# Kernel optimization log

Hardware: AMD Instinct MI355X
Metric: run time of the kernel (lower is better)

Reference implementation:

```python
import jax, jax.numpy as jnp
import numpy as np

B, V = 8, 60000

def _embed(x, n):
    # NeRF positional encoding: [x, sin(x*2^0), cos(x*2^0), ..., sin(x*2^{n-1}), cos(x*2^{n-1})]
    f = 2.0 ** jnp.arange(n, dtype=x.dtype)
    xf = x[..., None, :] * f[:, None]                      # [..., n, D]
    sc = jnp.stack([jnp.sin(xf), jnp.cos(xf)], axis=-2)    # [..., n, 2, D] (per-freq sin/cos interleave)
    return jnp.concatenate([x, sc.reshape(x.shape[:-1] + (-1,))], axis=-1)

def _mlp(x, params):
    for W, b in params[:-1]:
        x = jax.nn.silu(x @ W.T + b)
    W, b = params[-1]
    return x @ W.T + b

def _rx(a):
    c, s = jnp.cos(a), jnp.sin(a)
    o, z = jnp.ones_like(a), jnp.zeros_like(a)
    return jnp.stack([jnp.stack([o, z, z], -1), jnp.stack([z, c, -s], -1), jnp.stack([z, s, c], -1)], -2)

def _ry(a):
    c, s = jnp.cos(a), jnp.sin(a)
    o, z = jnp.ones_like(a), jnp.zeros_like(a)
    return jnp.stack([jnp.stack([c, z, s], -1), jnp.stack([z, o, z], -1), jnp.stack([-s, z, c], -1)], -2)

def _rz(a):
    c, s = jnp.cos(a), jnp.sin(a)
    o, z = jnp.ones_like(a), jnp.zeros_like(a)
    return jnp.stack([jnp.stack([c, -s, z], -1), jnp.stack([s, c, z], -1), jnp.stack([z, z, o], -1)], -2)

def _forward(vertices, features, ew0, eb0, ew1, eb1, ew2, eb2, ew3, eb3, ew4, eb4, ew5, eb5,
             tw0, tb0, tw1, tb1, tw2, tb2, tw3, tb3,
             pw0, pb0, pw1, pb1, pw2, pb2, pw3, pb3,
             transform_origin, scale):
    enc_v = _embed(vertices, 6)                            # [V, 78]
    enc_ov = _embed(vertices[:, :3], 3)                    # [V, 21]
    tmpl = _mlp(enc_ov, [(tw0, tb0), (tw1, tb1), (tw2, tb2), (tw3, tb3)])  # [V, 3]
    di = jnp.concatenate([jnp.broadcast_to(enc_v[None], (B, V, enc_v.shape[-1])),
                          jnp.broadcast_to(features[:, None, :53], (B, V, 53))], -1)  # [B,V,131]
    expr = _mlp(di, [(ew0, eb0), (ew1, eb1), (ew2, eb2), (ew3, eb3), (ew4, eb4), (ew5, eb5)])  # [B,V,3]
    ev = vertices[None, :, :3] + expr + tmpl[None]         # [B, V, 3]
    pi = jnp.concatenate([jnp.broadcast_to(enc_ov[None], (B, V, enc_ov.shape[-1])),
                          jnp.broadcast_to(features[:, None, 53:59], (B, V, 6))], -1)  # [B,V,27]
    w = jax.nn.sigmoid(_mlp(pi, [(pw0, pb0), (pw1, pb1), (pw2, pb2), (pw3, pb3)]))  # [B,V,1]
    ang = features[:, None, 53:56] * w                     # [B,V,3] per-vertex scaled euler angles
    # pytorch3d euler_angles_to_matrix, convention 'XYZ': R = R_X @ R_Y @ R_Z
    R = _rx(ang[..., 0]) @ _ry(ang[..., 1]) @ _rz(ang[..., 2])  # [B,V,3,3]
    origin = transform_origin * 0.1
    local = (ev - origin) * scale
    return jnp.einsum('bvd,bvdj->bvj', local, R) + features[:, None, 56:59] + origin

def _lin(key, fi, fo):
    # mimics xavier_uniform_(gain=0.1) + zero bias
    lim = 0.1 * np.sqrt(6.0 / (fi + fo))
    W = jax.random.uniform(key, (fo, fi), minval=-lim, maxval=lim, dtype=jnp.float32)
    return W, jnp.zeros((fo,), jnp.float32)

def setup_inputs():
    key = jax.random.key(0)
    ks = jax.random.split(key, 20)
    d = {}
    d['vertices'] = jax.random.normal(ks[0], (V, 6), jnp.float32)
    d['features'] = jax.random.normal(ks[1], (B, 62), jnp.float32) * 0.3
    exp_dims = [(131, 256), (256, 256), (256, 128), (128, 128), (128, 128), (128, 3)]
    for i, (fi, fo) in enumerate(exp_dims):
        d['ew%d' % i], d['eb%d' % i] = _lin(ks[2 + i], fi, fo)
    tmpl_dims = [(21, 64), (64, 32), (32, 32), (32, 3)]
    for i, (fi, fo) in enumerate(tmpl_dims):
        d['tw%d' % i], d['tb%d' % i] = _lin(ks[8 + i], fi, fo)
    pose_dims = [(27, 64), (64, 32), (32, 32), (32, 1)]
    for i, (fi, fo) in enumerate(pose_dims):
        d['pw%d' % i], d['pb%d' % i] = _lin(ks[12 + i], fi, fo)
    d['transform_origin'] = jnp.zeros((3,), jnp.float32)
    d['scale'] = jnp.ones((1,), jnp.float32)
    return d

def reference(vertices, features, ew0, eb0, ew1, eb1, ew2, eb2, ew3, eb3, ew4, eb4, ew5, eb5,
              tw0, tb0, tw1, tb1, tw2, tb2, tw3, tb3,
              pw0, pb0, pw1, pb1, pw2, pb2, pw3, pb3,
              transform_origin, scale):
    return _forward(vertices, features, ew0, eb0, ew1, eb1, ew2, eb2, ew3, eb3, ew4, eb4, ew5, eb5,
                    tw0, tb0, tw1, tb1, tw2, tb2, tw3, tb3,
                    pw0, pb0, pw1, pb1, pw2, pb2, pw3, pb3,
                    transform_origin, scale)
```

## Files before the change

kernel.cpp:

```cpp
#include <hip/hip_runtime.h>
#include <hip/hip_bf16.h>
#include <math.h>

#define V_TOT 60000
#define VPB 8
#define NBLK (V_TOT / VPB)

typedef short  s16x8 __attribute__((ext_vector_type(8)));
typedef float  f32x4 __attribute__((ext_vector_type(4)));

#define WS_EW0 0
#define WS_EW1 40960
#define WS_EW2 106496
#define WS_EW3 139264
#define WS_EW4 155648
#define WS_EW5 172032
#define WS_PW0 174080
#define WS_PW1 176128
#define WS_PW2 178176
#define WS_PW3 179200
#define WS_TW0 179712
#define WS_TW1 181760
#define WS_TW2 183808
#define WS_TW3 184832

#define L_ACTA 0
#define L_ENCF 0
#define L_OENC 2560
#define L_ACTB 33792
#define L_PH0  33792
#define L_PH1  43008
#define L_PH2  48128
#define L_A0P  67584
#define L_A0T  71680
#define L_TA   72704
#define L_TB   75008
#define L_TC   76288
#define L_FEAT 77568
#define L_VERT 79552
#define L_EXPR 79744
#define L_TMPL 80512
#define L_POSW 80608
#define SMEM_BYTES 80864

struct Params {
  const float* vertices; const float* features;
  const float* eb0; const float* eb1; const float* eb2; const float* eb3;
  const float* eb4; const float* eb5;
  const float* tb0; const float* tb1; const float* tb2; const float* tb3;
  const float* pb0; const float* pb1; const float* pb2; const float* pb3;
  const float* torigin; const float* scale;
  const ushort* wsb;
  float* out;
};

__device__ __forceinline__ float silu_f(float x) {
  float e = __expf(-x);
  return x * __builtin_amdgcn_rcpf(1.f + e);
}
__device__ __forceinline__ float sigm_f(float x) {
  return __builtin_amdgcn_rcpf(1.f + __expf(-x));
}
__device__ __forceinline__ ushort f2bf(float f) {
  unsigned u = __float_as_uint(f);
  return (ushort)((u + 0x7fffu + ((u >> 16) & 1u)) >> 16);
}
__device__ __forceinline__ unsigned pack2bf(float a, float b) {
  __hip_bfloat162 h = __float22bfloat162_rn(float2{a, b});
  unsigned u; __builtin_memcpy(&u, &h, 4); return u;
}

template<int KS, int SLOTS, int INSTR, int OUTSTR>
__device__ __forceinline__ void big_layer_T(const ushort* __restrict__ Wt,
                                            const float* __restrict__ bias,
                                            const ushort* inb, ushort* outb,
                                            int lane, int wv)
{
  const int r16 = lane & 15, g = lane >> 4;
  f32x4 acc[SLOTS][4];
  #pragma unroll
  for (int s = 0; s < SLOTS; s++) {
    const int nt = wv + s * 8;
    const float4 bv = *(const float4*)(bias + nt * 16 + g * 4);
    #pragma unroll
    for (int mt = 0; mt < 4; mt++) acc[s][mt] = (f32x4){bv.x, bv.y, bv.z, bv.w};
  }
  #pragma unroll
  for (int k = 0; k < KS; k++) {
    s16x8 bf[4];
    #pragma unroll
    for (int mt = 0; mt < 4; mt++)
      bf[mt] = *(const s16x8*)(inb + (mt * 16 + r16) * INSTR + k * 32 + g * 8);
    #pragma unroll
    for (int s = 0; s < SLOTS; s++) {
      const int nt = wv + s * 8;
      s16x8 aw = *(const s16x8*)(Wt + (size_t)(nt * KS + k) * 512 + lane * 8);
      #pragma unroll
      for (int mt = 0; mt < 4; mt++)
        acc[s][mt] = __builtin_amdgcn_mfma_f32_16x16x32_bf16(aw, bf[mt], acc[s][mt], 0, 0, 0);
    }
  }
  #pragma unroll
  for (int s = 0; s < SLOTS; s++) {
    const int nt = wv + s * 8;
    #pragma unroll
    for (int mt = 0; mt < 4; mt++) {
      uint2 w;
      w.x = pack2bf(silu_f(acc[s][mt][0]), silu_f(acc[s][mt][1]));
      w.y = pack2bf(silu_f(acc[s][mt][2]), silu_f(acc[s][mt][3]));
      *(uint2*)(outb + (mt * 16 + r16) * OUTSTR + nt * 16 + g * 4) = w;
    }
  }
}

template<int KS, int INSTR>
__device__ __forceinline__ f32x4 tile_mm_T(const ushort* __restrict__ Wt,
                                           const ushort* inb, int mt, int lane, f32x4 binit)
{
  const int r16 = lane & 15, g = lane >> 4;
  f32x4 acc = binit;
  #pragma unroll
  for (int k = 0; k < KS; k++) {
    s16x8 aw = *(const s16x8*)(Wt + k * 512 + lane * 8);
    s16x8 bf = *(const s16x8*)(inb + (mt * 16 + r16) * INSTR + k * 32 + g * 8);
    acc = __builtin_amdgcn_mfma_f32_16x16x32_bf16(aw, bf, acc, 0, 0, 0);
  }
  return acc;
}

__global__ void conv_w(const float* __restrict__ src, ushort* __restrict__ dst,
                       int NT, int KS, int Ksrc, int Kused, int Nused)
{
  int idx = blockIdx.x * 256 + threadIdx.x;
  if (idx >= NT * KS * 512) return;
  int t = idx >> 9, l = (idx >> 3) & 63, i = idx & 7;
  int nt = t / KS, k = t - nt * KS;
  int row = nt * 16 + (l & 15);
  int kk = k * 32 + (l >> 4) * 8 + i;
  float v = (row < Nused && kk < Kused) ? src[row * Ksrc + kk] : 0.f;
  dst[idx] = f2bf(v);
}

extern "C" __global__ __launch_bounds__(512, 4)
void nbs_kernel(Params P)
{
  extern __shared__ char sm[];
  ushort* actAb = (ushort*)(sm + L_ACTA);
  float*  encf  = (float*)(sm + L_ENCF);
  float*  oencf = (float*)(sm + L_OENC);
  ushort* a0    = (ushort*)(sm + L_ACTB);
  ushort* actBb = (ushort*)(sm + L_ACTB);
  ushort* ph0b  = (ushort*)(sm + L_PH0);
  ushort* ph1b  = (ushort*)(sm + L_PH1);
  ushort* ph2b  = (ushort*)(sm + L_PH2);
  ushort* a0p   = (ushort*)(sm + L_A0P);
  ushort* a0t   = (ushort*)(sm + L_A0T);
  ushort* tAl   = (ushort*)(sm + L_TA);
  ushort* tBl   = (ushort*)(sm + L_TB);
  ushort* tCl   = (ushort*)(sm + L_TC);
  float*  featl = (float*)(sm + L_FEAT);
  float*  vertl = (float*)(sm + L_VERT);
  float*  exprv = (float*)(sm + L_EXPR);
  float*  tmplv = (float*)(sm + L_TMPL);
  float*  posew = (float*)(sm + L_POSW);

  const int tid  = threadIdx.x;
  const int lane = tid & 63;
  const int wv   = __builtin_amdgcn_readfirstlane(tid >> 6);
  const int r16  = lane & 15, g = lane >> 4;
  const int v0   = blockIdx.x * VPB;
  const ushort* ws = P.wsb;

  for (int idx = tid; idx < 8 * 62; idx += 512) featl[idx] = P.features[idx];
  for (int idx = tid; idx < VPB * 6; idx += 512) vertl[idx] = P.vertices[(size_t)v0 * 6 + idx];
  __syncthreads();

  for (int idx = tid; idx < 8 * 80; idx += 512) {
    int v = idx / 80, e = idx - v * 80;
    float val = 0.f;
    if (e < 6) val = vertl[v * 6 + e];
    else if (e < 78) {
      int r = e - 6, k = r / 12, q = r - k * 12;
      float x = vertl[v * 6 + (q < 6 ? q : q - 6)] * (float)(1 << k);
      val = (q < 6) ? __sinf(x) : __cosf(x);
    }
    encf[idx] = val;
  }
  for (int idx = tid; idx < 8 * 24; idx += 512) {
    int v = idx / 24, e = idx - v * 24;
    float val = 0.f;
    if (e < 3) val = vertl[v * 6 + e];
    else if (e < 21) {
      int r = e - 3, k = r / 6, q = r - k * 6;
      float x = vertl[v * 6 + (q < 3 ? q : q - 3)] * (float)(1 << k);
      val = (q < 3) ? __sinf(x) : __cosf(x);
    }
    oencf[idx] = val;
  }
  __syncthreads();

  {
    uint* a0u = (uint*)a0;
    for (int idx = tid; idx < 64 * 80; idx += 512) {
      int p = idx / 80, q = idx - p * 80, vl = p >> 3, b = p & 7;
      int e0 = q * 2, e1 = e0 + 1;
      float s0 = (e0 < 78) ? encf[vl * 80 + e0] : (e0 < 131 ? featl[b * 62 + e0 - 78] : 0.f);
      float s1 = (e1 < 78) ? encf[vl * 80 + e1] : (e1 < 131 ? featl[b * 62 + e1 - 78] : 0.f);
      a0u[p * 80 + q] = pack2bf(s0, s1);
    }
    uint* a0pu = (uint*)a0p;
    for (int idx = tid; idx < 64 * 16; idx += 512) {
      int p = idx >> 4, q = idx & 15, vl = p >> 3, b = p & 7;
      int e0 = q * 2, e1 = e0 + 1;
      float s0 = (e0 < 21) ? oencf[vl * 24 + e0] : (e0 < 27 ? featl[b * 62 + 53 + e0 - 21] : 0.f);
      float s1 = (e1 < 21) ? oencf[vl * 24 + e1] : (e1 < 27 ? featl[b * 62 + 53 + e1 - 21] : 0.f);
      a0pu[p * 16 + q] = pack2bf(s0, s1);
    }
    uint* a0tu = (uint*)a0t;
    for (int idx = tid; idx < 16 * 16; idx += 512) {
      int v = idx >> 4, q = idx & 15;
      int e0 = q * 2, e1 = e0 + 1;
      float s0 = (v < 8 && e0 < 21) ? oencf[v * 24 + e0] : 0.f;
      float s1 = (v < 8 && e1 < 21) ? oencf[v * 24 + e1] : 0.f;
      a0tu[v * 16 + q] = pack2bf(s0, s1);
    }
  }
  __syncthreads();

  big_layer_T<5, 2, 160, 264>(ws + WS_EW0, P.eb0, a0,    actAb, lane, wv);
  __syncthreads();
  big_layer_T<8, 2, 264, 264>(ws + WS_EW1, P.eb1, actAb, actBb, lane, wv);
  __syncthreads();
  big_layer_T<8, 1, 264, 264>(ws + WS_EW2, P.eb2, actBb, actAb, lane, wv);
  __syncthreads();
  big_layer_T<4, 1, 264, 264>(ws + WS_EW3, P.eb3, actAb, actBb, lane, wv);
  __syncthreads();
  big_layer_T<4, 1, 264, 264>(ws + WS_EW4, P.eb4, actBb, actAb, lane, wv);
  __syncthreads();

  if (wv < 4) {
    const int nt = wv;
    const float4 bv = *(const float4*)(P.pb0 + nt * 16 + g * 4);
    #pragma unroll
    for (int mt = 0; mt < 4; mt++) {
      f32x4 d = tile_mm_T<1, 32>(ws + WS_PW0 + nt * 512, a0p, mt, lane,
                                 (f32x4){bv.x, bv.y, bv.z, bv.w});
      uint2 w;
      w.x = pack2bf(silu_f(d[0]), silu_f(d[1]));
      w.y = pack2bf(silu_f(d[2]), silu_f(d[3]));
      *(uint2*)(ph0b + (mt * 16 + r16) * 72 + nt * 16 + g * 4) = w;
    }
  } else {
    const int nt = wv - 4;
    const float4 bv = *(const float4*)(P.tb0 + nt * 16 + g * 4);
    f32x4 d = tile_mm_T<1, 32>(ws + WS_TW0 + nt * 512, a0t, 0, lane,
                               (f32x4){bv.x, bv.y, bv.z, bv.w});
    uint2 w;
    w.x = pack2bf(silu_f(d[0]), silu_f(d[1]));
    w.y = pack2bf(silu_f(d[2]), silu_f(d[3]));
    *(uint2*)(tAl + r16 * 72 + nt * 16 + g * 4) = w;
  }
  __syncthreads();

  if (wv >= 4) {
    const int mt = wv - 4;
    f32x4 bi = (f32x4){0.f, 0.f, 0.f, 0.f};
    if (g == 0) bi = (f32x4){P.eb5[0], P.eb5[1], P.eb5[2], 0.f};
    f32x4 d = tile_mm_T<4, 264>(ws + WS_EW5, actAb, mt, lane, bi);
    if (g == 0) {
      exprv[(mt * 16 + r16) * 3 + 0] = d[0];
      exprv[(mt * 16 + r16) * 3 + 1] = d[1];
      exprv[(mt * 16 + r16) * 3 + 2] = d[2];
    }
  } else if (wv < 2) {
    const int nt = wv;
    const float4 bv = *(const float4*)(P.pb1 + nt * 16 + g * 4);
    #pragma unroll
    for (int mt = 0; mt < 4; mt++) {
      f32x4 d = tile_mm_T<2, 72>(ws + WS_PW1 + nt * 2 * 512, ph0b, mt, lane,
                                 (f32x4){bv.x, bv.y, bv.z, bv.w});
      uint2 w;
      w.x = pack2bf(silu_f(d[0]), silu_f(d[1]));
      w.y = pack2bf(silu_f(d[2]), silu_f(d[3]));
      *(uint2*)(ph1b + (mt * 16 + r16) * 40 + nt * 16 + g * 4) = w;
    }
  } else {
    const int nt = wv - 2;
    const float4 bv = *(const float4*)(P.tb1 + nt * 16 + g * 4);
    f32x4 d = tile_mm_T<2, 72>(ws + WS_TW1 + nt * 2 * 512, tAl, 0, lane,
                               (f32x4){bv.x, bv.y, bv.z, bv.w});
    uint2 w;
    w.x = pack2bf(silu_f(d[0]), silu_f(d[1]));
    w.y = pack2bf(silu_f(d[2]), silu_f(d[3]));
    *(uint2*)(tBl + r16 * 40 + nt * 16 + g * 4) = w;
  }
  __syncthreads();

  if (wv < 2) {
    const int nt = wv;
    const float4 bv = *(const float4*)(P.pb2 + nt * 16 + g * 4);
    #pragma unroll
    for (int mt = 0; mt < 4; mt++) {
      f32x4 d = tile_mm_T<1, 40>(ws + WS_PW2 + nt * 512, ph1b, mt, lane,
                                 (f32x4){bv.x, bv.y, bv.z, bv.w});
      uint2 w;
      w.x = pack2bf(silu_f(d[0]), silu_f(d[1]));
      w.y = pack2bf(silu_f(d[2]), silu_f(d[3]));
      *(uint2*)(ph2b + (mt * 16 + r16) * 40 + nt * 16 + g * 4) = w;
    }
  } else if (wv == 2) {
    #pragma unroll
    for (int nt = 0; nt < 2; nt++) {
      const float4 bv = *(const float4*)(P.tb2 + nt * 16 + g * 4);
      f32x4 d = tile_mm_T<1, 40>(ws + WS_TW2 + nt * 512, tBl, 0, lane,
                                 (f32x4){bv.x, bv.y, bv.z, bv.w});
      uint2 w;
      w.x = pack2bf(silu_f(d[0]), silu_f(d[1]));
      w.y = pack2bf(silu_f(d[2]), silu_f(d[3]));
      *(uint2*)(tCl + r16 * 40 + nt * 16 + g * 4) = w;
    }
  }
  __syncthreads();

  if (wv == 0) {
    f32x4 bi = (g == 0) ? (f32x4){P.pb3[0], 0.f, 0.f, 0.f} : (f32x4){0.f, 0.f, 0.f, 0.f};
    #pragma unroll
    for (int mt = 0; mt < 4; mt++) {
      f32x4 d = tile_mm_T<1, 40>(ws + WS_PW3, ph2b, mt, lane, bi);
      if (g == 0) posew[mt * 16 + r16] = sigm_f(d[0]);
    }
  } else if (wv == 1) {
    f32x4 bi = (g == 0) ? (f32x4){P.tb3[0], P.tb3[1], P.tb3[2], 0.f}
                        : (f32x4){0.f, 0.f, 0.f, 0.f};
    f32x4 d = tile_mm_T<1, 40>(ws + WS_TW3, tCl, 0, lane, bi);
    if (g == 0 && r16 < 8) {
      tmplv[r16 * 3 + 0] = d[0];
      tmplv[r16 * 3 + 1] = d[1];
      tmplv[r16 * 3 + 2] = d[2];
    }
  }
  __syncthreads();

  if (tid < 64) {
    int p = tid, vl = p >> 3, b = p & 7;
    float ox = P.torigin[0] * 0.1f, oy = P.torigin[1] * 0.1f, oz = P.torigin[2] * 0.1f;
    float sc = P.scale[0];
    float ev0 = vertl[vl * 6 + 0] + exprv[p * 3 + 0] + tmplv[vl * 3 + 0];
    float ev1 = vertl[vl * 6 + 1] + exprv[p * 3 + 1] + tmplv[vl * 3 + 1];
    float ev2 = vertl[vl * 6 + 2] + exprv[p * 3 + 2] + tmplv[vl * 3 + 2];
    float w = posew[p];
    float a0a = featl[b * 62 + 53] * w;
    float a1a = featl[b * 62 + 54] * w;
    float a2a = featl[b * 62 + 55] * w;
    float c1 = __cosf(a0a), s1 = __sinf(a0a);
    float c2 = __cosf(a1a), s2 = __sinf(a1a);
    float c3 = __cosf(a2a), s3 = __sinf(a2a);
    float R00 = c2 * c3,                R01 = -c2 * s3,                R02 = s2;
    float R10 = c1 * s3 + s1 * s2 * c3, R11 = c1 * c3 - s1 * s2 * s3,  R12 = -s1 * c2;
    float R20 = s1 * s3 - c1 * s2 * c3, R21 = s1 * c3 + c1 * s2 * s3,  R22 = c1 * c2;
    float l0 = (ev0 - ox) * sc, l1 = (ev1 - oy) * sc, l2 = (ev2 - oz) * sc;
    float o0 = l0 * R00 + l1 * R10 + l2 * R20 + featl[b * 62 + 56] + ox;
    float o1 = l0 * R01 + l1 * R11 + l2 * R21 + featl[b * 62 + 57] + oy;
    float o2 = l0 * R02 + l1 * R12 + l2 * R22 + featl[b * 62 + 58] + oz;
    size_t o = ((size_t)b * V_TOT + (v0 + vl)) * 3;
    P.out[o + 0] = o0; P.out[o + 1] = o1; P.out[o + 2] = o2;
  }
}

extern "C" void kernel_launch(void* const* d_in, const int* in_sizes, int n_in,
                              void* d_out, int out_size, void* d_ws, size_t ws_size,
                              hipStream_t stream)
{
  (void)in_sizes; (void)n_in; (void)out_size; (void)ws_size;
  ushort* wsp = (ushort*)d_ws;

  auto L = [&](const void* s, int woff, int NT, int KS, int Ksrc, int Kused, int Nused) {
    int n = NT * KS * 512;
    hipLaunchKernelGGL(conv_w, dim3((n + 255) / 256), dim3(256), 0, stream,
                       (const float*)s, wsp + woff, NT, KS, Ksrc, Kused, Nused);
  };
  L(d_in[2],  WS_EW0, 16, 5, 131, 131, 256);
  L(d_in[4],  WS_EW1, 16, 8, 256, 256, 256);
  L(d_in[6],  WS_EW2,  8, 8, 256, 256, 128);
  L(d_in[8],  WS_EW3,  8, 4, 128, 128, 128);
  L(d_in[10], WS_EW4,  8, 4, 128, 128, 128);
  L(d_in[12], WS_EW5,  1, 4, 128, 128, 3);
  L(d_in[22], WS_PW0,  4, 1,  27,  27, 64);
  L(d_in[24], WS_PW1,  2, 2,  64,  64, 32);
  L(d_in[26], WS_PW2,  2, 1,  32,  32, 32);
  L(d_in[28], WS_PW3,  1, 1,  32,  32, 1);
  L(d_in[14], WS_TW0,  4, 1,  21,  21, 64);
  L(d_in[16], WS_TW1,  2, 2,  64,  64, 32);
  L(d_in[18], WS_TW2,  2, 1,  32,  32, 32);
  L(d_in[20], WS_TW3,  1, 1,  32,  32, 3);

  Params P;
  P.vertices = (const float*)d_in[0];  P.features = (const float*)d_in[1];
  P.eb0 = (const float*)d_in[3];   P.eb1 = (const float*)d_in[5];
  P.eb2 = (const float*)d_in[7];   P.eb3 = (const float*)d_in[9];
  P.eb4 = (const float*)d_in[11];  P.eb5 = (const float*)d_in[13];
  P.tb0 = (const float*)d_in[15];  P.tb1 = (const float*)d_in[17];
  P.tb2 = (const float*)d_in[19];  P.tb3 = (const float*)d_in[21];
  P.pb0 = (const float*)d_in[23];  P.pb1 = (const float*)d_in[25];
  P.pb2 = (const float*)d_in[27];  P.pb3 = (const float*)d_in[29];
  P.torigin = (const float*)d_in[30];
  P.scale   = (const float*)d_in[31];
  P.wsb = (const ushort*)wsp;
  P.out = (float*)d_out;

  (void)hipFuncSetAttribute((const void*)nbs_kernel,
                            hipFuncAttributeMaxDynamicSharedMemorySize, SMEM_BYTES);
  hipLaunchKernelGGL(nbs_kernel, dim3(NBLK), dim3(512), SMEM_BYTES, stream, P);
}
```

Baseline: 320.4 us.

## Halve vertices per block, shrink LDS, and rebalance MFMA tiles across waves

```diff
diff --git a/kernel.cpp b/kernel.cpp
--- a/kernel.cpp
+++ b/kernel.cpp
@@ -3,7 +3,7 @@
 #include <math.h>
 
 #define V_TOT 60000
-#define VPB 8
+#define VPB 4
 #define NBLK (V_TOT / VPB)
 
 typedef short  s16x8 __attribute__((ext_vector_type(8)));
@@ -26,22 +26,22 @@
 
 #define L_ACTA 0
 #define L_ENCF 0
-#define L_OENC 2560
-#define L_ACTB 33792
-#define L_PH0  33792
-#define L_PH1  43008
-#define L_PH2  48128
-#define L_A0P  67584
-#define L_A0T  71680
-#define L_TA   72704
-#define L_TB   75008
-#define L_TC   76288
-#define L_FEAT 77568
-#define L_VERT 79552
-#define L_EXPR 79744
-#define L_TMPL 80512
-#define L_POSW 80608
-#define SMEM_BYTES 80864
+#define L_OENC 1280
+#define L_ACTB 16896
+#define L_PH0  16896
+#define L_PH1  21504
+#define L_PH2  24064
+#define L_A0P  33792
+#define L_TB   33792
+#define L_A0T  35840
+#define L_TA   36864
+#define L_TC   36864
+#define L_VERT 39168
+#define L_FEATB 39264
+#define L_EXPR 40288
+#define L_TMPL 40672
+#define L_POSW 40720
+#define SMEM_BYTES 40848
 
 struct Params {
   const float* vertices; const float* features;
@@ -70,46 +70,41 @@
   unsigned u; __builtin_memcpy(&u, &h, 4); return u;
 }
 
-template<int KS, int SLOTS, int INSTR, int OUTSTR>
+template<int KS, int NT_TOT, int INSTR, int OUTSTR>
 __device__ __forceinline__ void big_layer_T(const ushort* __restrict__ Wt,
                                             const float* __restrict__ bias,
                                             const ushort* inb, ushort* outb,
                                             int lane, int wv)
 {
+  constexpr int SLOTS = NT_TOT / 4;
   const int r16 = lane & 15, g = lane >> 4;
-  f32x4 acc[SLOTS][4];
+  const int mt = wv & 1;
+  const ushort* ab = inb + (mt * 16 + r16) * INSTR + g * 8;
+  const ushort* wb[SLOTS];
+  f32x4 acc[SLOTS];
   #pragma unroll
   for (int s = 0; s < SLOTS; s++) {
-    const int nt = wv + s * 8;
+    const int nt = (wv >> 1) + s * 4;
+    wb[s] = Wt + (size_t)nt * KS * 512 + lane * 8;
     const float4 bv = *(const float4*)(bias + nt * 16 + g * 4);
-    #pragma unroll
-    for (int mt = 0; mt < 4; mt++) acc[s][mt] = (f32x4){bv.x, bv.y, bv.z, bv.w};
+    acc[s] = (f32x4){bv.x, bv.y, bv.z, bv.w};
   }
   #pragma unroll
   for (int k = 0; k < KS; k++) {
-    s16x8 bf[4];
-    #pragma unroll
-    for (int mt = 0; mt < 4; mt++)
-      bf[mt] = *(const s16x8*)(inb + (mt * 16 + r16) * INSTR + k * 32 + g * 8);
+    s16x8 bf = *(const s16x8*)(ab + k * 32);
     #pragma unroll
     for (int s = 0; s < SLOTS; s++) {
-      const int nt = wv + s * 8;
-      s16x8 aw = *(const s16x8*)(Wt + (size_t)(nt * KS + k) * 512 + lane * 8);
-      #pragma unroll
-      for (int mt = 0; mt < 4; mt++)
-        acc[s][mt] = __builtin_amdgcn_mfma_f32_16x16x32_bf16(aw, bf[mt], acc[s][mt], 0, 0, 0);
+      s16x8 aw = *(const s16x8*)(wb[s] + k * 512);
+      acc[s] = __builtin_amdgcn_mfma_f32_16x16x32_bf16(aw, bf, acc[s], 0, 0, 0);
     }
   }
   #pragma unroll
   for (int s = 0; s < SLOTS; s++) {
-    const int nt = wv + s * 8;
-    #pragma unroll
-    for (int mt = 0; mt < 4; mt++) {
-      uint2 w;
-      w.x = pack2bf(silu_f(acc[s][mt][0]), silu_f(acc[s][mt][1]));
-      w.y = pack2bf(silu_f(acc[s][mt][2]), silu_f(acc[s][mt][3]));
-      *(uint2*)(outb + (mt * 16 + r16) * OUTSTR + nt * 16 + g * 4) = w;
-    }
+    const int nt = (wv >> 1) + s * 4;
+    uint2 w;
+    w.x = pack2bf(silu_f(acc[s][0]), silu_f(acc[s][1]));
+    w.y = pack2bf(silu_f(acc[s][2]), silu_f(acc[s][3]));
+    *(uint2*)(outb + (mt * 16 + r16) * OUTSTR + nt * 16 + g * 4) = w;
   }
 }
 
@@ -141,7 +136,7 @@
   dst[idx] = f2bf(v);
 }
 
-extern "C" __global__ __launch_bounds__(512, 4)
+extern "C" __global__ __launch_bounds__(512, 8)
 void nbs_kernel(Params P)
 {
   extern __shared__ char sm[];
@@ -158,8 +153,8 @@
   ushort* tAl   = (ushort*)(sm + L_TA);
   ushort* tBl   = (ushort*)(sm + L_TB);
   ushort* tCl   = (ushort*)(sm + L_TC);
-  float*  featl = (float*)(sm + L_FEAT);
   float*  vertl = (float*)(sm + L_VERT);
+  ushort* featb = (ushort*)(sm + L_FEATB);
   float*  exprv = (float*)(sm + L_EXPR);
   float*  tmplv = (float*)(sm + L_TMPL);
   float*  posew = (float*)(sm + L_POSW);
@@ -171,78 +166,97 @@
   const int v0   = blockIdx.x * VPB;
   const ushort* ws = P.wsb;
 
-  for (int idx = tid; idx < 8 * 62; idx += 512) featl[idx] = P.features[idx];
-  for (int idx = tid; idx < VPB * 6; idx += 512) vertl[idx] = P.vertices[(size_t)v0 * 6 + idx];
-  __syncthreads();
-
-  for (int idx = tid; idx < 8 * 80; idx += 512) {
-    int v = idx / 80, e = idx - v * 80;
-    float val = 0.f;
-    if (e < 6) val = vertl[v * 6 + e];
-    else if (e < 78) {
-      int r = e - 6, k = r / 12, q = r - k * 12;
-      float x = vertl[v * 6 + (q < 6 ? q : q - 6)] * (float)(1 << k);
-      val = (q < 6) ? __sinf(x) : __cosf(x);
-    }
-    encf[idx] = val;
-  }
-  for (int idx = tid; idx < 8 * 24; idx += 512) {
-    int v = idx / 24, e = idx - v * 24;
-    float val = 0.f;
-    if (e < 3) val = vertl[v * 6 + e];
-    else if (e < 21) {
-      int r = e - 3, k = r / 6, q = r - k * 6;
-      float x = vertl[v * 6 + (q < 3 ? q : q - 3)] * (float)(1 << k);
-      val = (q < 3) ? __sinf(x) : __cosf(x);
-    }
-    oencf[idx] = val;
+  {
+    uint* fbu = (uint*)featb;
+    if (tid < 256) {
+      int b = tid >> 5, q = tid & 31;
+      int e0 = q * 2, e1 = e0 + 1;
+      float s0 = (e0 < 62) ? P.features[b * 62 + e0] : 0.f;
+      float s1 = (e1 < 62) ? P.features[b * 62 + e1] : 0.f;
+      fbu[b * 32 + q] = pack2bf(s0, s1);
+    }
+    if (tid < VPB * 6) vertl[tid] = P.vertices[(size_t)v0 * 6 + tid];
+    int i2 = tid - 256;
+    if (i2 >= 0 && i2 < 4 * 80) {
+      int v = i2 / 80, e = i2 - v * 80;
+      float val = 0.f;
+      if (e < 6) val = P.vertices[(size_t)(v0 + v) * 6 + e];
+      else if (e < 78) {
+        int r = e - 6, k = r / 12, q = r - k * 12;
+        float x = P.vertices[(size_t)(v0 + v) * 6 + (q < 6 ? q : q - 6)] * (float)(1 << k);
+        val = (q < 6) ? __sinf(x) : __cosf(x);
+      }
+      encf[i2] = val;
+    }
+    int i3 = tid - (256 + 320);
+    if (i3 >= 0 && i3 < 4 * 24) {
+      int v = i3 / 24, e = i3 - v * 24;
+      float val = 0.f;
+      if (e < 3) val = P.vertices[(size_t)(v0 + v) * 6 + e];
+      else if (e < 21) {
+        int r = e - 3, k = r / 6, q = r - k * 6;
+        float x = P.vertices[(size_t)(v0 + v) * 6 + (q < 3 ? q : q - 3)] * (float)(1 << k);
+        val = (q < 3) ? __sinf(x) : __cosf(x);
+      }
+      oencf[i3] = val;
+    }
   }
   __syncthreads();
 
   {
     uint* a0u = (uint*)a0;
-    for (int idx = tid; idx < 64 * 80; idx += 512) {
+    uint* fbu = (uint*)featb;
+    ushort* fbs = featb;
+    for (int idx = tid; idx < 32 * 80; idx += 512) {
       int p = idx / 80, q = idx - p * 80, vl = p >> 3, b = p & 7;
-      int e0 = q * 2, e1 = e0 + 1;
-      float s0 = (e0 < 78) ? encf[vl * 80 + e0] : (e0 < 131 ? featl[b * 62 + e0 - 78] : 0.f);
-      float s1 = (e1 < 78) ? encf[vl * 80 + e1] : (e1 < 131 ? featl[b * 62 + e1 - 78] : 0.f);
-      a0u[p * 80 + q] = pack2bf(s0, s1);
+      uint u;
+      if (q < 39)       u = pack2bf(encf[vl * 80 + 2 * q], encf[vl * 80 + 2 * q + 1]);
+      else if (q < 65)  u = fbu[b * 32 + (q - 39)];
+      else if (q == 65) u = (uint)fbs[b * 64 + 52];
+      else              u = 0u;
+      a0u[p * 80 + q] = u;
     }
     uint* a0pu = (uint*)a0p;
-    for (int idx = tid; idx < 64 * 16; idx += 512) {
-      int p = idx >> 4, q = idx & 15, vl = p >> 3, b = p & 7;
-      int e0 = q * 2, e1 = e0 + 1;
-      float s0 = (e0 < 21) ? oencf[vl * 24 + e0] : (e0 < 27 ? featl[b * 62 + 53 + e0 - 21] : 0.f);
-      float s1 = (e1 < 21) ? oencf[vl * 24 + e1] : (e1 < 27 ? featl[b * 62 + 53 + e1 - 21] : 0.f);
-      a0pu[p * 16 + q] = pack2bf(s0, s1);
+    if (tid < 512) {
+      int p = tid >> 4, q = tid & 15, vl = p >> 3, b = p & 7;
+      uint u;
+      if (q < 10)       u = pack2bf(oencf[vl * 24 + 2 * q], oencf[vl * 24 + 2 * q + 1]);
+      else if (q == 10) u = (uint)f2bf(oencf[vl * 24 + 20]) | ((uint)fbs[b * 64 + 53] << 16);
+      else if (q == 11) u = fbu[b * 32 + 27];
+      else if (q == 12) u = fbu[b * 32 + 28];
+      else if (q == 13) u = (uint)fbs[b * 64 + 58];
+      else              u = 0u;
+      a0pu[p * 16 + q] = u;
     }
     uint* a0tu = (uint*)a0t;
-    for (int idx = tid; idx < 16 * 16; idx += 512) {
-      int v = idx >> 4, q = idx & 15;
-      int e0 = q * 2, e1 = e0 + 1;
-      float s0 = (v < 8 && e0 < 21) ? oencf[v * 24 + e0] : 0.f;
-      float s1 = (v < 8 && e1 < 21) ? oencf[v * 24 + e1] : 0.f;
-      a0tu[v * 16 + q] = pack2bf(s0, s1);
-    }
-  }
-  __syncthreads();
-
-  big_layer_T<5, 2, 160, 264>(ws + WS_EW0, P.eb0, a0,    actAb, lane, wv);
-  __syncthreads();
-  big_layer_T<8, 2, 264, 264>(ws + WS_EW1, P.eb1, actAb, actBb, lane, wv);
-  __syncthreads();
-  big_layer_T<8, 1, 264, 264>(ws + WS_EW2, P.eb2, actBb, actAb, lane, wv);
-  __syncthreads();
-  big_layer_T<4, 1, 264, 264>(ws + WS_EW3, P.eb3, actAb, actBb, lane, wv);
-  __syncthreads();
-  big_layer_T<4, 1, 264, 264>(ws + WS_EW4, P.eb4, actBb, actAb, lane, wv);
+    if (tid < 256) {
+      int v = tid >> 4, q = tid & 15;
+      uint u = 0u;
+      if (v < 4) {
+        if (q < 10)       u = pack2bf(oencf[v * 24 + 2 * q], oencf[v * 24 + 2 * q + 1]);
+        else if (q == 10) u = (uint)f2bf(oencf[v * 24 + 20]);
+      }
+      a0tu[v * 16 + q] = u;
+    }
+  }
+  __syncthreads();
+
+  big_layer_T<5, 16, 160, 264>(ws + WS_EW0, P.eb0, a0,    actAb, lane, wv);
+  __syncthreads();
+  big_layer_T<8, 16, 264, 264>(ws + WS_EW1, P.eb1, actAb, actBb, lane, wv);
+  __syncthreads();
+  big_layer_T<8,  8, 264, 264>(ws + WS_EW2, P.eb2, actBb, actAb, lane, wv);
+  __syncthreads();
+  big_layer_T<4,  8, 264, 264>(ws + WS_EW3, P.eb3, actAb, actBb, lane, wv);
+  __syncthreads();
+  big_layer_T<4,  8, 264, 264>(ws + WS_EW4, P.eb4, actBb, actAb, lane, wv);
   __syncthreads();
 
   if (wv < 4) {
     const int nt = wv;
     const float4 bv = *(const float4*)(P.pb0 + nt * 16 + g * 4);
     #pragma unroll
-    for (int mt = 0; mt < 4; mt++) {
+    for (int mt = 0; mt < 2; mt++) {
       f32x4 d = tile_mm_T<1, 32>(ws + WS_PW0 + nt * 512, a0p, mt, lane,
                                  (f32x4){bv.x, bv.y, bv.z, bv.w});
       uint2 w;
@@ -262,7 +276,16 @@
   }
   __syncthreads();
 
-  if (wv >= 4) {
+  if (wv < 4) {
+    const int nt = wv >> 1, mt = wv & 1;
+    const float4 bv = *(const float4*)(P.pb1 + nt * 16 + g * 4);
+    f32x4 d = tile_mm_T<2, 72>(ws + WS_PW1 + nt * 2 * 512, ph0b, mt, lane,
+                               (f32x4){bv.x, bv.y, bv.z, bv.w});
+    uint2 w;
+    w.x = pack2bf(silu_f(d[0]), silu_f(d[1]));
+    w.y = pack2bf(silu_f(d[2]), silu_f(d[3]));
+    *(uint2*)(ph1b + (mt * 16 + r16) * 40 + nt * 16 + g * 4) = w;
+  } else if (wv < 6) {
     const int mt = wv - 4;
     f32x4 bi = (f32x4){0.f, 0.f, 0.f, 0.f};
     if (g == 0) bi = (f32x4){P.eb5[0], P.eb5[1], P.eb5[2], 0.f};
@@ -272,20 +295,8 @@
       exprv[(mt * 16 + r16) * 3 + 1] = d[1];
       exprv[(mt * 16 + r16) * 3 + 2] = d[2];
     }
-  } else if (wv < 2) {
-    const int nt = wv;
-    const float4 bv = *(const float4*)(P.pb1 + nt * 16 + g * 4);
-    #pragma unroll
-    for (int mt = 0; mt < 4; mt++) {
-      f32x4 d = tile_mm_T<2, 72>(ws + WS_PW1 + nt * 2 * 512, ph0b, mt, lane,
-                                 (f32x4){bv.x, bv.y, bv.z, bv.w});
-      uint2 w;
-      w.x = pack2bf(silu_f(d[0]), silu_f(d[1]));
-      w.y = pack2bf(silu_f(d[2]), silu_f(d[3]));
-      *(uint2*)(ph1b + (mt * 16 + r16) * 40 + nt * 16 + g * 4) = w;
-    }
   } else {
-    const int nt = wv - 2;
+    const int nt = wv - 6;
     const float4 bv = *(const float4*)(P.tb1 + nt * 16 + g * 4);
     f32x4 d = tile_mm_T<2, 72>(ws + WS_TW1 + nt * 2 * 512, tAl, 0, lane,
                                (f32x4){bv.x, bv.y, bv.z, bv.w});
@@ -296,44 +307,37 @@
   }
   __syncthreads();
 
+  if (wv < 4) {
+    const int nt = wv >> 1, mt = wv & 1;
+    const float4 bv = *(const float4*)(P.pb2 + nt * 16 + g * 4);
+    f32x4 d = tile_mm_T<1, 40>(ws + WS_PW2 + nt * 512, ph1b, mt, lane,
+                               (f32x4){bv.x, bv.y, bv.z, bv.w});
+    uint2 w;
+    w.x = pack2bf(silu_f(d[0]), silu_f(d[1]));
+    w.y = pack2bf(silu_f(d[2]), silu_f(d[3]));
+    *(uint2*)(ph2b + (mt * 16 + r16) * 40 + nt * 16 + g * 4) = w;
+  } else if (wv < 6) {
+    const int nt = wv - 4;
+    const float4 bv = *(const float4*)(P.tb2 + nt * 16 + g * 4);
+    f32x4 d = tile_mm_T<1, 40>(ws + WS_TW2 + nt * 512, tBl, 0, lane,
+                               (f32x4){bv.x, bv.y, bv.z, bv.w});
+    uint2 w;
+    w.x = pack2bf(silu_f(d[0]), silu_f(d[1]));
+    w.y = pack2bf(silu_f(d[2]), silu_f(d[3]));
+    *(uint2*)(tCl + r16 * 40 + nt * 16 + g * 4) = w;
+  }
+  __syncthreads();
+
   if (wv < 2) {
-    const int nt = wv;
-    const float4 bv = *(const float4*)(P.pb2 + nt * 16 + g * 4);
-    #pragma unroll
-    for (int mt = 0; mt < 4; mt++) {
-      f32x4 d = tile_mm_T<1, 40>(ws + WS_PW2 + nt * 512, ph1b, mt, lane,
-                                 (f32x4){bv.x, bv.y, bv.z, bv.w});
-      uint2 w;
-      w.x = pack2bf(silu_f(d[0]), silu_f(d[1]));
-      w.y = pack2bf(silu_f(d[2]), silu_f(d[3]));
-      *(uint2*)(ph2b + (mt * 16 + r16) * 40 + nt * 16 + g * 4) = w;
-    }
+    const int mt = wv;
+    f32x4 bi = (g == 0) ? (f32x4){P.pb3[0], 0.f, 0.f, 0.f} : (f32x4){0.f, 0.f, 0.f, 0.f};
+    f32x4 d = tile_mm_T<1, 40>(ws + WS_PW3, ph2b, mt, lane, bi);
+    if (g == 0) posew[mt * 16 + r16] = sigm_f(d[0]);
   } else if (wv == 2) {
-    #pragma unroll
-    for (int nt = 0; nt < 2; nt++) {
-      const float4 bv = *(const float4*)(P.tb2 + nt * 16 + g * 4);
-      f32x4 d = tile_mm_T<1, 40>(ws + WS_TW2 + nt * 512, tBl, 0, lane,
-                                 (f32x4){bv.x, bv.y, bv.z, bv.w});
-      uint2 w;
-      w.x = pack2bf(silu_f(d[0]), silu_f(d[1]));
-      w.y = pack2bf(silu_f(d[2]), silu_f(d[3]));
-      *(uint2*)(tCl + r16 * 40 + nt * 16 + g * 4) = w;
-    }
-  }
-  __syncthreads();
-
-  if (wv == 0) {
-    f32x4 bi = (g == 0) ? (f32x4){P.pb3[0], 0.f, 0.f, 0.f} : (f32x4){0.f, 0.f, 0.f, 0.f};
-    #pragma unroll
-    for (int mt = 0; mt < 4; mt++) {
-      f32x4 d = tile_mm_T<1, 40>(ws + WS_PW3, ph2b, mt, lane, bi);
-      if (g == 0) posew[mt * 16 + r16] = sigm_f(d[0]);
-    }
-  } else if (wv == 1) {
     f32x4 bi = (g == 0) ? (f32x4){P.tb3[0], P.tb3[1], P.tb3[2], 0.f}
                         : (f32x4){0.f, 0.f, 0.f, 0.f};
     f32x4 d = tile_mm_T<1, 40>(ws + WS_TW3, tCl, 0, lane, bi);
-    if (g == 0 && r16 < 8) {
+    if (g == 0 && r16 < 4) {
       tmplv[r16 * 3 + 0] = d[0];
       tmplv[r16 * 3 + 1] = d[1];
       tmplv[r16 * 3 + 2] = d[2];
@@ -341,7 +345,7 @@
   }
   __syncthreads();
 
-  if (tid < 64) {
+  if (tid < 32) {
     int p = tid, vl = p >> 3, b = p & 7;
     float ox = P.torigin[0] * 0.1f, oy = P.torigin[1] * 0.1f, oz = P.torigin[2] * 0.1f;
     float sc = P.scale[0];
@@ -349,9 +353,10 @@
     float ev1 = vertl[vl * 6 + 1] + exprv[p * 3 + 1] + tmplv[vl * 3 + 1];
     float ev2 = vertl[vl * 6 + 2] + exprv[p * 3 + 2] + tmplv[vl * 3 + 2];
     float w = posew[p];
-    float a0a = featl[b * 62 + 53] * w;
-    float a1a = featl[b * 62 + 54] * w;
-    float a2a = featl[b * 62 + 55] * w;
+    const float* fb = P.features + b * 62;
+    float a0a = fb[53] * w;
+    float a1a = fb[54] * w;
+    float a2a = fb[55] * w;
     float c1 = __cosf(a0a), s1 = __sinf(a0a);
     float c2 = __cosf(a1a), s2 = __sinf(a1a);
     float c3 = __cosf(a2a), s3 = __sinf(a2a);
@@ -359,9 +364,9 @@
     float R10 = c1 * s3 + s1 * s2 * c3, R11 = c1 * c3 - s1 * s2 * s3,  R12 = -s1 * c2;
     float R20 = s1 * s3 - c1 * s2 * c3, R21 = s1 * c3 + c1 * s2 * s3,  R22 = c1 * c2;
     float l0 = (ev0 - ox) * sc, l1 = (ev1 - oy) * sc, l2 = (ev2 - oz) * sc;
-    float o0 = l0 * R00 + l1 * R10 + l2 * R20 + featl[b * 62 + 56] + ox;
-    float o1 = l0 * R01 + l1 * R11 + l2 * R21 + featl[b * 62 + 57] + oy;
-    float o2 = l0 * R02 + l1 * R12 + l2 * R22 + featl[b * 62 + 58] + oz;
+    float o0 = l0 * R00 + l1 * R10 + l2 * R20 + fb[56] + ox;
+    float o1 = l0 * R01 + l1 * R11 + l2 * R21 + fb[57] + oy;
+    float o2 = l0 * R02 + l1 * R12 + l2 * R22 + fb[58] + oz;
     size_t o = ((size_t)b * V_TOT + (v0 + vl)) * 3;
     P.out[o + 0] = o0; P.out[o + 1] = o1; P.out[o + 2] = o2;
   }
```

After: 412.1 us. 28.6% more time.

## Split first expression layer into per-vertex and per-batch parts, shrink LDS

Applied to the files above, without the earlier changes.

```diff
diff --git a/kernel.cpp b/kernel.cpp
--- a/kernel.cpp
+++ b/kernel.cpp
@@ -23,34 +23,34 @@
 #define WS_TW1 181760
 #define WS_TW2 183808
 #define WS_TW3 184832
-
-#define L_ACTA 0
-#define L_ENCF 0
-#define L_OENC 2560
-#define L_ACTB 33792
-#define L_PH0  33792
-#define L_PH1  43008
-#define L_PH2  48128
-#define L_A0P  67584
-#define L_A0T  71680
-#define L_TA   72704
-#define L_TB   75008
-#define L_TC   76288
-#define L_FEAT 77568
-#define L_VERT 79552
-#define L_EXPR 79744
-#define L_TMPL 80512
-#define L_POSW 80608
-#define SMEM_BYTES 80864
+#define WS_F   185344
+
+#define L_ACT   0
+#define L_U     33792
+#define L_ENC96 42112
+#define L_OENC  45184
+#define L_A0P   33792
+#define L_A0T   37888
+#define L_TA    38912
+#define L_TB    41216
+#define L_TC    42496
+#define L_FEATB 45952
+#define L_VERT  46976
+#define L_EXPR  47168
+#define L_TMPL  47936
+#define L_POSW  48032
+#define SMEM_BYTES 48288
 
 struct Params {
-  const float* vertices; const float* features;
-  const float* eb0; const float* eb1; const float* eb2; const float* eb3;
-  const float* eb4; const float* eb5;
+  const float* features;
+  const float* vertices;
+  const float* eb1; const float* eb2; const float* eb3; const float* eb4;
+  const float* eb5;
   const float* tb0; const float* tb1; const float* tb2; const float* tb3;
   const float* pb0; const float* pb1; const float* pb2; const float* pb3;
   const float* torigin; const float* scale;
   const ushort* wsb;
+  const float* Fg;
   float* out;
 };
 
@@ -70,12 +70,13 @@
   unsigned u; __builtin_memcpy(&u, &h, 4); return u;
 }
 
-template<int KS, int SLOTS, int INSTR, int OUTSTR>
+template<int KS, int NT_TOT, int INSTR, int OUTSTR>
 __device__ __forceinline__ void big_layer_T(const ushort* __restrict__ Wt,
                                             const float* __restrict__ bias,
                                             const ushort* inb, ushort* outb,
                                             int lane, int wv)
 {
+  constexpr int SLOTS = NT_TOT / 8;
   const int r16 = lane & 15, g = lane >> 4;
   f32x4 acc[SLOTS][4];
   #pragma unroll
@@ -100,6 +101,7 @@
         acc[s][mt] = __builtin_amdgcn_mfma_f32_16x16x32_bf16(aw, bf[mt], acc[s][mt], 0, 0, 0);
     }
   }
+  __syncthreads();
   #pragma unroll
   for (int s = 0; s < SLOTS; s++) {
     const int nt = wv + s * 8;
@@ -141,28 +143,41 @@
   dst[idx] = f2bf(v);
 }
 
-extern "C" __global__ __launch_bounds__(512, 4)
+__global__ void calc_F(const float* __restrict__ feats, const float* __restrict__ ew0,
+                       const float* __restrict__ eb0, float* __restrict__ Fout)
+{
+  int t = threadIdx.x;
+  int b = t >> 5, j0 = (t & 31) * 8;
+  for (int jj = 0; jj < 8; jj++) {
+    int j = j0 + jj;
+    float acc = eb0[j];
+    const float* Wr = ew0 + (size_t)j * 131 + 78;
+    for (int i = 0; i < 53; i++) acc = fmaf(feats[b * 62 + i], Wr[i], acc);
+    Fout[b * 256 + j] = acc;
+  }
+}
+
+extern "C" __global__ __launch_bounds__(512, 6)
 void nbs_kernel(Params P)
 {
   extern __shared__ char sm[];
-  ushort* actAb = (ushort*)(sm + L_ACTA);
-  float*  encf  = (float*)(sm + L_ENCF);
-  float*  oencf = (float*)(sm + L_OENC);
-  ushort* a0    = (ushort*)(sm + L_ACTB);
-  ushort* actBb = (ushort*)(sm + L_ACTB);
-  ushort* ph0b  = (ushort*)(sm + L_PH0);
-  ushort* ph1b  = (ushort*)(sm + L_PH1);
-  ushort* ph2b  = (ushort*)(sm + L_PH2);
-  ushort* a0p   = (ushort*)(sm + L_A0P);
-  ushort* a0t   = (ushort*)(sm + L_A0T);
-  ushort* tAl   = (ushort*)(sm + L_TA);
-  ushort* tBl   = (ushort*)(sm + L_TB);
-  ushort* tCl   = (ushort*)(sm + L_TC);
-  float*  featl = (float*)(sm + L_FEAT);
-  float*  vertl = (float*)(sm + L_VERT);
-  float*  exprv = (float*)(sm + L_EXPR);
-  float*  tmplv = (float*)(sm + L_TMPL);
-  float*  posew = (float*)(sm + L_POSW);
+  ushort* actAb  = (ushort*)(sm + L_ACT);
+  float*  U      = (float*)(sm + L_U);
+  ushort* enc96b = (ushort*)(sm + L_ENC96);
+  float*  oencf  = (float*)(sm + L_OENC);
+  ushort* a0p    = (ushort*)(sm + L_A0P);
+  ushort* a0t    = (ushort*)(sm + L_A0T);
+  ushort* tAl    = (ushort*)(sm + L_TA);
+  ushort* tBl    = (ushort*)(sm + L_TB);
+  ushort* tCl    = (ushort*)(sm + L_TC);
+  ushort* featb  = (ushort*)(sm + L_FEATB);
+  float*  vertl  = (float*)(sm + L_VERT);
+  float*  exprv  = (float*)(sm + L_EXPR);
+  float*  tmplv  = (float*)(sm + L_TMPL);
+  float*  posew  = (float*)(sm + L_POSW);
+  ushort* ph0b = actAb + 132;
+  ushort* ph1b = actAb + 204;
+  ushort* ph2b = actAb + 132;
 
   const int tid  = threadIdx.x;
   const int lane = tid & 63;
@@ -171,71 +186,115 @@
   const int v0   = blockIdx.x * VPB;
   const ushort* ws = P.wsb;
 
-  for (int idx = tid; idx < 8 * 62; idx += 512) featl[idx] = P.features[idx];
-  for (int idx = tid; idx < VPB * 6; idx += 512) vertl[idx] = P.vertices[(size_t)v0 * 6 + idx];
-  __syncthreads();
-
-  for (int idx = tid; idx < 8 * 80; idx += 512) {
-    int v = idx / 80, e = idx - v * 80;
-    float val = 0.f;
-    if (e < 6) val = vertl[v * 6 + e];
-    else if (e < 78) {
-      int r = e - 6, k = r / 12, q = r - k * 12;
-      float x = vertl[v * 6 + (q < 6 ? q : q - 6)] * (float)(1 << k);
-      val = (q < 6) ? __sinf(x) : __cosf(x);
-    }
-    encf[idx] = val;
-  }
-  for (int idx = tid; idx < 8 * 24; idx += 512) {
-    int v = idx / 24, e = idx - v * 24;
-    float val = 0.f;
-    if (e < 3) val = vertl[v * 6 + e];
-    else if (e < 21) {
-      int r = e - 3, k = r / 6, q = r - k * 6;
-      float x = vertl[v * 6 + (q < 3 ? q : q - 3)] * (float)(1 << k);
-      val = (q < 3) ? __sinf(x) : __cosf(x);
-    }
-    oencf[idx] = val;
-  }
-  __syncthreads();
-
   {
-    uint* a0u = (uint*)a0;
-    for (int idx = tid; idx < 64 * 80; idx += 512) {
-      int p = idx / 80, q = idx - p * 80, vl = p >> 3, b = p & 7;
+    uint* fbu = (uint*)featb;
+    if (tid < 256) {
+      int b = tid >> 5, q = tid & 31;
       int e0 = q * 2, e1 = e0 + 1;
-      float s0 = (e0 < 78) ? encf[vl * 80 + e0] : (e0 < 131 ? featl[b * 62 + e0 - 78] : 0.f);
-      float s1 = (e1 < 78) ? encf[vl * 80 + e1] : (e1 < 131 ? featl[b * 62 + e1 - 78] : 0.f);
-      a0u[p * 80 + q] = pack2bf(s0, s1);
-    }
+      float s0 = (e0 < 62) ? P.features[b * 62 + e0] : 0.f;
+      float s1 = (e1 < 62) ? P.features[b * 62 + e1] : 0.f;
+      fbu[b * 32 + q] = pack2bf(s0, s1);
+    }
+    if (tid < VPB * 6) vertl[tid] = P.vertices[(size_t)v0 * 6 + tid];
+    int i2 = tid - 256;
+    if (i2 >= 0 && i2 < 16 * 48) {
+      int v = i2 / 48, q = i2 - v * 48;
+      float s[2];
+      #pragma unroll
+      for (int h = 0; h < 2; h++) {
+        int e = q * 2 + h;
+        float val = 0.f;
+        if (v < 8) {
+          if (e < 6) val = P.vertices[(size_t)(v0 + v) * 6 + e];
+          else if (e < 78) {
+            int r = e - 6, k = r / 12, qq = r - k * 12;
+            float x = P.vertices[(size_t)(v0 + v) * 6 + (qq < 6 ? qq : qq - 6)] * (float)(1 << k);
+            val = (qq < 6) ? __sinf(x) : __cosf(x);
+          }
+        }
+        s[h] = val;
+      }
+      ((uint*)enc96b)[v * 48 + q] = pack2bf(s[0], s[1]);
+    }
+    int i3 = tid - 64;
+    if (i3 >= 0 && i3 < 8 * 24) {
+      int v = i3 / 24, e = i3 - v * 24;
+      float val = 0.f;
+      if (e < 3) val = P.vertices[(size_t)(v0 + v) * 6 + e];
+      else if (e < 21) {
+        int r = e - 3, k = r / 6, q = r - k * 6;
+        float x = P.vertices[(size_t)(v0 + v) * 6 + (q < 3 ? q : q - 3)] * (float)(1 << k);
+        val = (q < 3) ? __sinf(x) : __cosf(x);
+      }
+      oencf[i3] = val;
+    }
+  }
+  __syncthreads();
+
+  {
+    #pragma unroll
+    for (int s = 0; s < 2; s++) {
+      const int nt = wv + s * 8;
+      f32x4 acc = (f32x4){0.f, 0.f, 0.f, 0.f};
+      #pragma unroll
+      for (int k = 0; k < 3; k++) {
+        s16x8 aw = *(const s16x8*)(ws + WS_EW0 + (size_t)(nt * 3 + k) * 512 + lane * 8);
+        s16x8 bf = *(const s16x8*)(enc96b + r16 * 96 + k * 32 + g * 8);
+        acc = __builtin_amdgcn_mfma_f32_16x16x32_bf16(aw, bf, acc, 0, 0, 0);
+      }
+      if (r16 < 8) *(f32x4*)(U + r16 * 260 + nt * 16 + g * 4) = acc;
+    }
+  }
+  __syncthreads();
+
+  {
+    f32x4 u4 = *(const f32x4*)(U + wv * 260 + lane * 4);
+    #pragma unroll 1
+    for (int b = 0; b < 8; b++) {
+      float4 f4 = *(const float4*)(P.Fg + b * 256 + lane * 4);
+      uint2 w;
+      w.x = pack2bf(silu_f(u4[0] + f4.x), silu_f(u4[1] + f4.y));
+      w.y = pack2bf(silu_f(u4[2] + f4.z), silu_f(u4[3] + f4.w));
+      *(uint2*)(actAb + (wv * 8 + b) * 264 + lane * 4) = w;
+    }
+  }
+  __syncthreads();
+
+  big_layer_T<8, 16, 264, 264>(ws + WS_EW1, P.eb1, actAb, actAb, lane, wv);
+  __syncthreads();
+  big_layer_T<8,  8, 264, 264>(ws + WS_EW2, P.eb2, actAb, actAb, lane, wv);
+  __syncthreads();
+  big_layer_T<4,  8, 264, 264>(ws + WS_EW3, P.eb3, actAb, actAb, lane, wv);
+  __syncthreads();
+  big_layer_T<4,  8, 264, 264>(ws + WS_EW4, P.eb4, actAb, actAb, lane, wv);
+  __syncthreads();
+
+  {
     uint* a0pu = (uint*)a0p;
+    ushort* fbs = featb;
+    uint* fbu = (uint*)featb;
     for (int idx = tid; idx < 64 * 16; idx += 512) {
       int p = idx >> 4, q = idx & 15, vl = p >> 3, b = p & 7;
-      int e0 = q * 2, e1 = e0 + 1;
-      float s0 = (e0 < 21) ? oencf[vl * 24 + e0] : (e0 < 27 ? featl[b * 62 + 53 + e0 - 21] : 0.f);
-      float s1 = (e1 < 21) ? oencf[vl * 24 + e1] : (e1 < 27 ? featl[b * 62 + 53 + e1 - 21] : 0.f);
-      a0pu[p * 16 + q] = pack2bf(s0, s1);
+      uint u;
+      if (q < 10)       u = pack2bf(oencf[vl * 24 + 2 * q], oencf[vl * 24 + 2 * q + 1]);
+      else if (q == 10) u = (uint)f2bf(oencf[vl * 24 + 20]) | ((uint)fbs[b * 64 + 53] << 16);
+      else if (q == 11) u = fbu[b * 32 + 27];
+      else if (q == 12) u = fbu[b * 32 + 28];
+      else if (q == 13) u = (uint)fbs[b * 64 + 58];
+      else              u = 0u;
+      a0pu[p * 16 + q] = u;
     }
     uint* a0tu = (uint*)a0t;
-    for (int idx = tid; idx < 16 * 16; idx += 512) {
-      int v = idx >> 4, q = idx & 15;
-      int e0 = q * 2, e1 = e0 + 1;
-      float s0 = (v < 8 && e0 < 21) ? oencf[v * 24 + e0] : 0.f;
-      float s1 = (v < 8 && e1 < 21) ? oencf[v * 24 + e1] : 0.f;
-      a0tu[v * 16 + q] = pack2bf(s0, s1);
-    }
-  }
-  __syncthreads();
-
-  big_layer_T<5, 2, 160, 264>(ws + WS_EW0, P.eb0, a0,    actAb, lane, wv);
-  __syncthreads();
-  big_layer_T<8, 2, 264, 264>(ws + WS_EW1, P.eb1, actAb, actBb, lane, wv);
-  __syncthreads();
-  big_layer_T<8, 1, 264, 264>(ws + WS_EW2, P.eb2, actBb, actAb, lane, wv);
-  __syncthreads();
-  big_layer_T<4, 1, 264, 264>(ws + WS_EW3, P.eb3, actAb, actBb, lane, wv);
-  __syncthreads();
-  big_layer_T<4, 1, 264, 264>(ws + WS_EW4, P.eb4, actBb, actAb, lane, wv);
+    if (tid < 256) {
+      int v = tid >> 4, q = tid & 15;
+      uint u = 0u;
+      if (v < 8) {
+        if (q < 10)       u = pack2bf(oencf[v * 24 + 2 * q], oencf[v * 24 + 2 * q + 1]);
+        else if (q == 10) u = (uint)f2bf(oencf[v * 24 + 20]);
+      }
+      a0tu[v * 16 + q] = u;
+    }
+  }
   __syncthreads();
 
   if (wv < 4) {
@@ -248,7 +307,7 @@
       uint2 w;
       w.x = pack2bf(silu_f(d[0]), silu_f(d[1]));
       w.y = pack2bf(silu_f(d[2]), silu_f(d[3]));
-      *(uint2*)(ph0b + (mt * 16 + r16) * 72 + nt * 16 + g * 4) = w;
+      *(uint2*)(ph0b + (mt * 16 + r16) * 264 + nt * 16 + g * 4) = w;
     }
   } else {
     const int nt = wv - 4;
@@ -277,12 +336,12 @@
     const float4 bv = *(const float4*)(P.pb1 + nt * 16 + g * 4);
     #pragma unroll
     for (int mt = 0; mt < 4; mt++) {
-      f32x4 d = tile_mm_T<2, 72>(ws + WS_PW1 + nt * 2 * 512, ph0b, mt, lane,
+      f32x4 d = tile_mm_T<2, 264>(ws + WS_PW1 + nt * 2 * 512, ph0b, mt, lane,
                                  (f32x4){bv.x, bv.y, bv.z, bv.w});
       uint2 w;
       w.x = pack2bf(silu_f(d[0]), silu_f(d[1]));
       w.y = pack2bf(silu_f(d[2]), silu_f(d[3]));
-      *(uint2*)(ph1b + (mt * 16 + r16) * 40 + nt * 16 + g * 4) = w;
+      *(uint2*)(ph1b + (mt * 16 + r16) * 264 + nt * 16 + g * 4) = w;
     }
   } else {
     const int nt = wv - 2;
@@ -296,29 +355,27 @@
   }
   __syncthreads();
 
-  if (wv < 2) {
-    const int nt = wv;
+  if (wv < 4) {
+    const int nt = wv >> 1, mt = (wv & 1) * 2;
     const float4 bv = *(const float4*)(P.pb2 + nt * 16 + g * 4);
     #pragma unroll
-    for (int mt = 0; mt < 4; mt++) {
-      f32x4 d = tile_mm_T<1, 40>(ws + WS_PW2 + nt * 512, ph1b, mt, lane,
+    for (int m = 0; m < 2; m++) {
+      f32x4 d = tile_mm_T<1, 264>(ws + WS_PW2 + nt * 512, ph1b, mt + m, lane,
                                  (f32x4){bv.x, bv.y, bv.z, bv.w});
       uint2 w;
       w.x = pack2bf(silu_f(d[0]), silu_f(d[1]));
       w.y = pack2bf(silu_f(d[2]), silu_f(d[3]));
-      *(uint2*)(ph2b + (mt * 16 + r16) * 40 + nt * 16 + g * 4) = w;
-    }
-  } else if (wv == 2) {
-    #pragma unroll
-    for (int nt = 0; nt < 2; nt++) {
-      const float4 bv = *(const float4*)(P.tb2 + nt * 16 + g * 4);
-      f32x4 d = tile_mm_T<1, 40>(ws + WS_TW2 + nt * 512, tBl, 0, lane,
-                                 (f32x4){bv.x, bv.y, bv.z, bv.w});
-      uint2 w;
-      w.x = pack2bf(silu_f(d[0]), silu_f(d[1]));
-      w.y = pack2bf(silu_f(d[2]), silu_f(d[3]));
-      *(uint2*)(tCl + r16 * 40 + nt * 16 + g * 4) = w;
-    }
+      *(uint2*)(ph2b + ((mt + m) * 16 + r16) * 264 + nt * 16 + g * 4) = w;
+    }
+  } else if (wv < 6) {
+    const int nt = wv - 4;
+    const float4 bv = *(const float4*)(P.tb2 + nt * 16 + g * 4);
+    f32x4 d = tile_mm_T<1, 40>(ws + WS_TW2 + nt * 512, tBl, 0, lane,
+                               (f32x4){bv.x, bv.y, bv.z, bv.w});
+    uint2 w;
+    w.x = pack2bf(silu_f(d[0]), silu_f(d[1]));
+    w.y = pack2bf(silu_f(d[2]), silu_f(d[3]));
+    *(uint2*)(tCl + r16 * 40 + nt * 16 + g * 4) = w;
   }
   __syncthreads();
 
@@ -326,7 +383,7 @@
     f32x4 bi = (g == 0) ? (f32x4){P.pb3[0], 0.f, 0.f, 0.f} : (f32x4){0.f, 0.f, 0.f, 0.f};
     #pragma unroll
     for (int mt = 0; mt < 4; mt++) {
-      f32x4 d = tile_mm_T<1, 40>(ws + WS_PW3, ph2b, mt, lane, bi);
+      f32x4 d = tile_mm_T<1, 264>(ws + WS_PW3, ph2b, mt, lane, bi);
       if (g == 0) posew[mt * 16 + r16] = sigm_f(d[0]);
     }
   } else if (wv == 1) {
@@ -349,9 +406,10 @@
     float ev1 = vertl[vl * 6 + 1] + exprv[p * 3 + 1] + tmplv[vl * 3 + 1];
     float ev2 = vertl[vl * 6 + 2] + exprv[p * 3 + 2] + tmplv[vl * 3 + 2];
     float w = posew[p];
-    float a0a = featl[b * 62 + 53] * w;
-    float a1a = featl[b * 62 + 54] * w;
-    float a2a = featl[b * 62 + 55] * w;
+    const float* fb = P.features + b * 62;
+    float a0a = fb[53] * w;
+    float a1a = fb[54] * w;
+    float a2a = fb[55] * w;
     float c1 = __cosf(a0a), s1 = __sinf(a0a);
     float c2 = __cosf(a1a), s2 = __sinf(a1a);
     float c3 = __cosf(a2a), s3 = __sinf(a2a);
@@ -359,9 +417,9 @@
     float R10 = c1 * s3 + s1 * s2 * c3, R11 = c1 * c3 - s1 * s2 * s3,  R12 = -s1 * c2;
     float R20 = s1 * s3 - c1 * s2 * c3, R21 = s1 * c3 + c1 * s2 * s3,  R22 = c1 * c2;
     float l0 = (ev0 - ox) * sc, l1 = (ev1 - oy) * sc, l2 = (ev2 - oz) * sc;
-    float o0 = l0 * R00 + l1 * R10 + l2 * R20 + featl[b * 62 + 56] + ox;
-    float o1 = l0 * R01 + l1 * R11 + l2 * R21 + featl[b * 62 + 57] + oy;
-    float o2 = l0 * R02 + l1 * R12 + l2 * R22 + featl[b * 62 + 58] + oz;
+    float o0 = l0 * R00 + l1 * R10 + l2 * R20 + fb[56] + ox;
+    float o1 = l0 * R01 + l1 * R11 + l2 * R21 + fb[57] + oy;
+    float o2 = l0 * R02 + l1 * R12 + l2 * R22 + fb[58] + oz;
     size_t o = ((size_t)b * V_TOT + (v0 + vl)) * 3;
     P.out[o + 0] = o0; P.out[o + 1] = o1; P.out[o + 2] = o2;
   }
@@ -373,13 +431,14 @@
 {
   (void)in_sizes; (void)n_in; (void)out_size; (void)ws_size;
   ushort* wsp = (ushort*)d_ws;
+  float*  Fws = (float*)(wsp + WS_F);
 
   auto L = [&](const void* s, int woff, int NT, int KS, int Ksrc, int Kused, int Nused) {
     int n = NT * KS * 512;
     hipLaunchKernelGGL(conv_w, dim3((n + 255) / 256), dim3(256), 0, stream,
                        (const float*)s, wsp + woff, NT, KS, Ksrc, Kused, Nused);
   };
-  L(d_in[2],  WS_EW0, 16, 5, 131, 131, 256);
+  L(d_in[2],  WS_EW0, 16, 3, 131,  78, 256);
   L(d_in[4],  WS_EW1, 16, 8, 256, 256, 256);
   L(d_in[6],  WS_EW2,  8, 8, 256, 256, 128);
   L(d_in[8],  WS_EW3,  8, 4, 128, 128, 128);
@@ -393,10 +452,14 @@
   L(d_in[16], WS_TW1,  2, 2,  64,  64, 32);
   L(d_in[18], WS_TW2,  2, 1,  32,  32, 32);
   L(d_in[20], WS_TW3,  1, 1,  32,  32, 3);
+  hipLaunchKernelGGL(calc_F, dim3(1), dim3(256), 0, stream,
+                     (const float*)d_in[1], (const float*)d_in[2],
+                     (const float*)d_in[3], Fws);
 
   Params P;
-  P.vertices = (const float*)d_in[0];  P.features = (const float*)d_in[1];
-  P.eb0 = (const float*)d_in[3];   P.eb1 = (const float*)d_in[5];
+  P.features = (const float*)d_in[1];
+  P.vertices = (const float*)d_in[0];
+  P.eb1 = (const float*)d_in[5];
   P.eb2 = (const float*)d_in[7];   P.eb3 = (const float*)d_in[9];
   P.eb4 = (const float*)d_in[11];  P.eb5 = (const float*)d_in[13];
   P.tb0 = (const float*)d_in[15];  P.tb1 = (const float*)d_in[17];
@@ -406,6 +469,7 @@
   P.torigin = (const float*)d_in[30];
   P.scale   = (const float*)d_in[31];
   P.wsb = (const ushort*)wsp;
+  P.Fg  = (const float*)Fws;
   P.out = (float*)d_out;
 
   (void)hipFuncSetAttribute((const void*)nbs_kernel,
```

Result: faster. 285.2 us (-11.0%).
